# Kernel optimization log

Measured on AMD Instinct MI355X. Metric: run time of the kernel, lower is better.

Reference implementation:

```python
import jax, jax.numpy as jnp
import numpy as np
from jax import lax

N, C_IN, DIMS, NW, T, H, W = 8, 64, 64, 8, 16, 64, 64
BN_EPS = 1e-5


def setup_inputs() -> dict:
    key = jax.random.key(0)
    ks = jax.random.split(key, 10)
    # kaiming-ish scales
    w_scale = (2.0 / (C_IN * 27)) ** 0.5
    return {
        "x": jax.random.normal(ks[0], (N, C_IN, T, H, W), dtype=jnp.float32),
        "weights": jax.random.normal(ks[1], (NW, DIMS, C_IN, 3, 3, 3), dtype=jnp.float32) * w_scale,
        "biases": jax.random.normal(ks[2], (NW, DIMS), dtype=jnp.float32),
        "se_w1": jax.random.normal(ks[3], (16, C_IN, 5, 5), dtype=jnp.float32) * (2.0 / (C_IN * 25)) ** 0.5,
        "se_b1": jnp.zeros((16,), dtype=jnp.float32),
        "se_w2": jax.random.normal(ks[4], (32, 16, 5, 5), dtype=jnp.float32) * (2.0 / (16 * 25)) ** 0.5,
        "se_b2": jnp.zeros((32,), dtype=jnp.float32),
        "lin_w": jax.random.normal(ks[5], (NW, 32), dtype=jnp.float32) * (1.0 / 32) ** 0.5,
        "lin_b": jnp.zeros((NW,), dtype=jnp.float32),
        "bn_gamma": jnp.ones((DIMS,), dtype=jnp.float32),
        "bn_beta": jnp.zeros((DIMS,), dtype=jnp.float32),
        "epochs_num": 15,
    }


def _forward(x, weights, biases, se_w1, se_b1, se_w2, se_b2, lin_w, lin_b, bn_gamma, bn_beta, epochs_num):
    tau = 30.0 - 2.9 * epochs_num if epochs_num < 10 else 1.0
    # std over temporal axis (torch.std -> unbiased, ddof=1): [n, c, h, w]
    std_x = jnp.std(x, axis=2, ddof=1)
    # squeeze-expand attention branch
    dn2d = ("NCHW", "OIHW", "NCHW")
    h1 = lax.conv_general_dilated(std_x, se_w1, (1, 1), "VALID", dimension_numbers=dn2d)
    h1 = jax.nn.relu(h1 + se_b1[None, :, None, None])
    h2 = lax.conv_general_dilated(h1, se_w2, (1, 1), "VALID", dimension_numbers=dn2d)
    h2 = jax.nn.relu(h2 + se_b2[None, :, None, None])
    pooled = jnp.max(h2, axis=(2, 3))                      # [n, 32]
    logits = pooled @ lin_w.T + lin_b                       # [n, num_weights]
    phi = jax.nn.softmax(logits / tau, axis=1)
    # per-sample dynamic kernels / biases
    dyn_w = jnp.einsum("bn,ncidhw->bcidhw", phi, weights)   # [n, dims, c_in, 3,3,3]
    dyn_b = phi @ biases                                    # [n, dims]
    # grouped conv3d (groups = n) == per-sample conv3d via vmap
    dn3d = ("NCDHW", "OIDHW", "NCDHW")
    def one_conv(xi, wi):
        return lax.conv_general_dilated(xi[None], wi, (1, 1, 1), "SAME", dimension_numbers=dn3d)[0]
    y = jax.vmap(one_conv)(x, dyn_w)                        # [n, dims, t, h, w]
    y = y + dyn_b[:, :, None, None, None]
    # BatchNorm3d (training mode, batch stats, biased var)
    mean = jnp.mean(y, axis=(0, 2, 3, 4))
    var = jnp.var(y, axis=(0, 2, 3, 4))
    b = lambda v: v[None, :, None, None, None]
    y = (y - b(mean)) * b(bn_gamma) * lax.rsqrt(b(var) + BN_EPS) + b(bn_beta)
    return jax.nn.relu(y)


def reference(x, weights, biases, se_w1, se_b1, se_w2, se_b2, lin_w, lin_b, bn_gamma, bn_beta, epochs_num):
    return _forward(x, weights, biases, se_w1, se_b1, se_w2, se_b2, lin_w, lin_b, bn_gamma, bn_beta, epochs_num)
```

## Files before the change

kernel.cpp:

```cpp
#include <hip/hip_runtime.h>
#include <hip/hip_bf16.h>
#include <math.h>

#define N_   8
#define CIN_ 64
#define DIMS_ 64
#define NW_  8
#define T_   16
#define H_   64
#define W_   64
#define HW_  (H_ * W_)
#define THW_ (T_ * HW_)

typedef short bf16x8 __attribute__((ext_vector_type(8)));
typedef float f32x16 __attribute__((ext_vector_type(16)));

__device__ __forceinline__ unsigned short f2bf(float f) {
    union { float f; unsigned u; } a; a.f = f;
    unsigned r = a.u + 0x7fffu + ((a.u >> 16) & 1u);
    return (unsigned short)(r >> 16);
}
__device__ __forceinline__ float bf2f(unsigned short u) {
    union { unsigned u; float f; } a; a.u = ((unsigned)u) << 16; return a.f;
}

#define CS8_ 8
#define HS8_ (66 * CS8_)
#define TS8_ (10 * HS8_)
#define XSH_ (3 * TS8_)

__host__ __device__ constexpr int OXc(int tap) {
    int tt = tap > 26 ? 26 : tap;
    return (tt / 9) * TS8_ + ((tt % 9) / 3) * HS8_ + ((tt % 3) - 1) * CS8_;
}

__global__ __launch_bounds__(512) void stdxb_kernel(
    const float* __restrict__ x, float* __restrict__ std_x,
    unsigned short* __restrict__ xb, float* __restrict__ sums,
    unsigned* __restrict__ pooled,
    const float* __restrict__ w1, const float* __restrict__ w2,
    float* __restrict__ w1t, float* __restrict__ w2t)
{
    __shared__ unsigned short xsl[16 * 64 * 8];
    const int h = blockIdx.x, c8 = blockIdx.y, n = blockIdx.z;
    const int tid = threadIdx.x;
    const int bf = blockIdx.x + (blockIdx.y << 6) + ((int)blockIdx.z << 9);
    if (bf == 0) {
        if (tid < 128) sums[tid] = 0.f;
        else if (tid < 384) pooled[tid - 128] = 0u;
    }
    if (bf < 75) {
        int i = bf * 512 + tid;
        if (i < 25600) {
            int k = i / 1600, c = (i / 25) % 64, tap = i % 25;
            w1t[(c * 25 + tap) * 16 + k] = w1[i];
        } else if (i < 38400) {
            int j = i - 25600;
            int o = j / 400, c = (j / 25) % 16, tap = j % 25;
            w2t[(c * 25 + tap) * 32 + o] = w2[j];
        }
    }
    const int c = tid >> 6, w = tid & 63;
    const int cin = c8 * 8 + c;
    const float* px = x + (((size_t)(n * 64 + cin)) << 16) + (h << 6) + w;
    float s = 0.f, s2 = 0.f;
#pragma unroll
    for (int t = 0; t < T_; ++t) {
        float v = px[t * HW_];
        s += v;
        s2 += v * v;
        xsl[(t << 9) + (w << 3) + c] = f2bf(v);
    }
    float var = (s2 - s * s * (1.0f / 16.0f)) * (1.0f / 15.0f);
    std_x[(((size_t)(n * 64 + cin)) << 12) + (h << 6) + w] = sqrtf(fmaxf(var, 0.f));
    __syncthreads();
    const int4* src = (const int4*)xsl;
    int4* dst = (int4*)(xb + ((size_t)((n * 8 + c8) * 16) << 12) * 8);
#pragma unroll
    for (int k = 0; k < 2; ++k) {
        int j = tid + (k << 9);
        int t = j >> 6, ww = j & 63;
        dst[((t << 6) + h) * 64 + ww] = src[j];
    }
}

__global__ __launch_bounds__(256) void se_conv1c(const float* __restrict__ std_x,
        const float* __restrict__ w1t, const float* __restrict__ b1, float* __restrict__ h1) {
    __shared__ float red[3][64][8];
    const int n = blockIdx.y, ks = blockIdx.z * 8;
    const int iq = threadIdx.x & 63, cq = threadIdx.x >> 6;
    const int ij = blockIdx.x * 64 + iq;
    float acc[8];
#pragma unroll
    for (int q = 0; q < 8; ++q) acc[q] = 0.f;
    if (ij < 3600) {
        int i = ij / 60, j = ij - i * 60;
        const float* xn = std_x + (size_t)n * CIN_ * HW_ + i * W_ + j;
        for (int c = cq * 16; c < cq * 16 + 16; ++c) {
            const float* xc = xn + c * HW_;
            float xv[25];
#pragma unroll
            for (int u = 0; u < 5; ++u)
#pragma unroll
                for (int v = 0; v < 5; ++v) xv[u * 5 + v] = xc[u * W_ + v];
            const float* wc = w1t + c * 400 + ks;
#pragma unroll
            for (int tap = 0; tap < 25; ++tap)
#pragma unroll
                for (int q = 0; q < 8; ++q)
                    acc[q] = fmaf(xv[tap], wc[tap * 16 + q], acc[q]);
        }
    }
    if (cq > 0) {
#pragma unroll
        for (int q = 0; q < 8; ++q) red[cq - 1][iq][q] = acc[q];
    }
    __syncthreads();
    if (cq == 0 && ij < 3600) {
#pragma unroll
        for (int q = 0; q < 8; ++q) {
            float a = acc[q] + red[0][iq][q] + red[1][iq][q] + red[2][iq][q] + b1[ks + q];
            h1[((size_t)(n * 16 + ks + q)) * 3600 + ij] = fmaxf(a, 0.f);
        }
    }
}

__global__ __launch_bounds__(256) void se_conv2c(const float* __restrict__ h1,
        const float* __restrict__ w2t, const float* __restrict__ b2,
        unsigned* __restrict__ pooled) {
    __shared__ float red[3][64][8];
    const int n = blockIdx.y, os = blockIdx.z * 8;
    const int iq = threadIdx.x & 63, cq = threadIdx.x >> 6;
    const int ij = blockIdx.x * 64 + iq;
    const int i = ij / 56, j = ij - i * 56;
    float acc[8];
#pragma unroll
    for (int q = 0; q < 8; ++q) acc[q] = 0.f;
    const float* xn = h1 + (size_t)n * 16 * 3600 + i * 60 + j;
    for (int c = cq * 4; c < cq * 4 + 4; ++c) {
        const float* xc = xn + c * 3600;
        float xv[25];
#pragma unroll
        for (int u = 0; u < 5; ++u)
#pragma unroll
            for (int v = 0; v < 5; ++v) xv[u * 5 + v] = xc[u * 60 + v];
        const float* wc = w2t + c * 800 + os;
#pragma unroll
        for (int tap = 0; tap < 25; ++tap)
#pragma unroll
            for (int q = 0; q < 8; ++q)
                acc[q] = fmaf(xv[tap], wc[tap * 32 + q], acc[q]);
    }
    if (cq > 0) {
#pragma unroll
        for (int q = 0; q < 8; ++q) red[cq - 1][iq][q] = acc[q];
    }
    __syncthreads();
    if (cq == 0) {
#pragma unroll
        for (int q = 0; q < 8; ++q) {
            float a = fmaxf(acc[q] + red[0][iq][q] + red[1][iq][q] + red[2][iq][q] + b2[os + q], 0.f);
#pragma unroll
            for (int m = 1; m < 64; m <<= 1) a = fmaxf(a, __shfl_xor(a, m, 64));
            if (iq == 0) atomicMax(&pooled[n * 32 + os + q], __float_as_uint(a));
        }
    }
}

__global__ __launch_bounds__(256) void dyn_w_head(
    const float* __restrict__ weights, const float* __restrict__ pooled,
    const float* __restrict__ lin_w, const float* __restrict__ lin_b,
    const float* __restrict__ biases, const int* __restrict__ epochs,
    unsigned short* __restrict__ wtb2, float* __restrict__ dyn_b) {
    __shared__ float slog[8][8];
    __shared__ float sphi[64];
    const int tid = threadIdx.x;
    const int e = epochs[0];
    const float tau = (e < 10) ? (30.0f - 2.9f * (float)e) : 1.0f;
    if (tid < 64) {
        int b = tid >> 3, m = tid & 7;
        float acc = lin_b[m];
#pragma unroll
        for (int k = 0; k < 32; ++k) acc += pooled[b * 32 + k] * lin_w[m * 32 + k];
        slog[b][m] = acc / tau;
    }
    __syncthreads();
    if (tid < 8) {
        float mx = slog[tid][0];
#pragma unroll
        for (int m = 1; m < 8; ++m) mx = fmaxf(mx, slog[tid][m]);
        float ex[8], ssum = 0.f;
#pragma unroll
        for (int m = 0; m < 8; ++m) { ex[m] = expf(slog[tid][m] - mx); ssum += ex[m]; }
        float inv = 1.0f / ssum;
#pragma unroll
        for (int m = 0; m < 8; ++m) sphi[tid * 8 + m] = ex[m] * inv;
    }
    __syncthreads();
    if (blockIdx.x < 64) {
        int b = blockIdx.x >> 3, c8 = blockIdx.x & 7;
        unsigned* dst = (unsigned*)(wtb2 + (size_t)b * 114688 + (size_t)(c8 * 28 + 27) * 512);
        dst[tid] = 0u;
    }
    if (blockIdx.x == 0) {
#pragma unroll
        for (int idx = tid; idx < 512; idx += 256) {
            int b = idx >> 6, d = idx & 63;
            float a = 0.f;
#pragma unroll
            for (int m = 0; m < 8; ++m) a += sphi[b * 8 + m] * biases[m * DIMS_ + d];
            dyn_b[idx] = a;
        }
    }
    int f = blockIdx.x * 256 + tid;
    if (f >= 110592) return;
    int tap = f % 27, cin = (f / 27) & 63, co = f / 1728;
    float wv[8];
#pragma unroll
    for (int m = 0; m < 8; ++m) wv[m] = weights[(size_t)m * 110592 + f];
    size_t dbase = (size_t)(cin >> 3) * 14336 + tap * 512 + co * 8 + (cin & 7);
#pragma unroll
    for (int b = 0; b < 8; ++b) {
        float acc = 0.f;
#pragma unroll
        for (int m = 0; m < 8; ++m) acc += sphi[b * 8 + m] * wv[m];
        wtb2[(size_t)b * 114688 + dbase] = f2bf(acc);
    }
}

__global__ __launch_bounds__(256, 2) void conv3d_mfma8(
    const unsigned short* __restrict__ xb,
    const unsigned short* __restrict__ wtb2,
    const float* __restrict__ dynb,
    float* __restrict__ y,
    unsigned short* __restrict__ ybf,
    float* __restrict__ sums)
{
    __shared__ __align__(16) unsigned short xs[XSH_];
    __shared__ float bnred[128];

    const int hb = blockIdx.x, t = blockIdx.y, n = blockIdx.z;
    const int tid = threadIdx.x;
    const int lane = tid & 63, wid = tid >> 6;
    const int lane31 = lane & 31, tau = lane >> 5;
    const int hbase = hb * 8;

    for (int i = tid; i < XSH_ / 8; i += 256)
        *(int4*)&xs[i * 8] = (int4){0, 0, 0, 0};
    if (tid < 128) bnred[tid] = 0.f;

    const unsigned short* xnb = xb + (size_t)n * 4194304;
    const unsigned short* wnb = wtb2 + (size_t)n * 114688;

    f32x16 acc[2][4];
#pragma unroll
    for (int ci = 0; ci < 2; ++ci)
#pragma unroll
        for (int s = 0; s < 4; ++s)
            acc[ci][s] = (f32x16)(0.f);

    const int aBase = tau * 512 + lane31 * 8;
    int bsp[4];
#pragma unroll
    for (int s = 0; s < 4; ++s)
        bsp[s] = (2 * wid + (s >> 1)) * HS8_ + (1 + (s & 1) * 32 + lane31) * CS8_;

    for (int c8 = 0; c8 < 8; ++c8) {
        __syncthreads();
#pragma unroll
        for (int k = 0; k < 8; ++k) {
            int r = wid + (k << 2);
            if (r < 30) {
                int tp = (r >= 20) ? 2 : (r >= 10 ? 1 : 0);
                int hp = r - tp * 10;
                int gt = t + tp - 1, gh = hbase + hp - 1;
                if (((unsigned)gt < 16u) && ((unsigned)gh < 64u)) {
                    const unsigned short* gp = xnb + (size_t)(((c8 * 16 + gt) * 64 + gh) * 64 + lane) * 8;
                    const unsigned short* lp = &xs[tp * TS8_ + hp * HS8_ + CS8_];
                    __builtin_amdgcn_global_load_lds(
                        (const __attribute__((address_space(1))) void*)gp,
                        (__attribute__((address_space(3))) void*)lp, 16, 0, 0);
                }
            }
        }
        __syncthreads();

        const unsigned short* wA = wnb + (size_t)c8 * 14336;
#pragma unroll
        for (int p = 0; p < 14; ++p) {
            const int xo = tau ? OXc(2 * p + 1) : OXc(2 * p);
            bf16x8 a0 = *(const bf16x8*)(wA + p * 1024 + aBase);
            bf16x8 a1 = *(const bf16x8*)(wA + p * 1024 + aBase + 256);
            bf16x8 b0 = *(const bf16x8*)&xs[bsp[0] + xo];
            bf16x8 b1 = *(const bf16x8*)&xs[bsp[1] + xo];
            bf16x8 b2 = *(const bf16x8*)&xs[bsp[2] + xo];
            bf16x8 b3 = *(const bf16x8*)&xs[bsp[3] + xo];
            acc[0][0] = __builtin_amdgcn_mfma_f32_32x32x16_bf16(a0, b0, acc[0][0], 0, 0, 0);
            acc[0][1] = __builtin_amdgcn_mfma_f32_32x32x16_bf16(a0, b1, acc[0][1], 0, 0, 0);
            acc[0][2] = __builtin_amdgcn_mfma_f32_32x32x16_bf16(a0, b2, acc[0][2], 0, 0, 0);
            acc[0][3] = __builtin_amdgcn_mfma_f32_32x32x16_bf16(a0, b3, acc[0][3], 0, 0, 0);
            acc[1][0] = __builtin_amdgcn_mfma_f32_32x32x16_bf16(a1, b0, acc[1][0], 0, 0, 0);
            acc[1][1] = __builtin_amdgcn_mfma_f32_32x32x16_bf16(a1, b1, acc[1][1], 0, 0, 0);
            acc[1][2] = __builtin_amdgcn_mfma_f32_32x32x16_bf16(a1, b2, acc[1][2], 0, 0, 0);
            acc[1][3] = __builtin_amdgcn_mfma_f32_32x32x16_bf16(a1, b3, acc[1][3], 0, 0, 0);
        }
    }

    const float* db = dynb + n * DIMS_;
    const bool bf = (ybf != nullptr);
#pragma unroll
    for (int ci = 0; ci < 2; ++ci) {
#pragma unroll
        for (int r = 0; r < 16; ++r) {
            const int co = 32 * ci + (r & 3) + 8 * (r >> 2) + 4 * tau;
            const float bco = db[co];
            float ps = 0.f, ps2 = 0.f;
#pragma unroll
            for (int s = 0; s < 4; ++s) {
                float z = acc[ci][s][r] + bco;
                size_t yi = ((size_t)(n * 64 + co) << 16) + ((size_t)t << 12)
                          + ((size_t)(hbase + 2 * wid + (s >> 1)) << 6) + (s & 1) * 32 + lane31;
                if (bf) ybf[yi] = f2bf(z);
                else    y[yi] = z;
                ps += z;
                ps2 += z * z;
            }
#pragma unroll
            for (int m = 1; m < 32; m <<= 1) {
                ps += __shfl_xor(ps, m, 64);
                ps2 += __shfl_xor(ps2, m, 64);
            }
            if (lane31 == 0) {
                atomicAdd(&bnred[co], ps);
                atomicAdd(&bnred[64 + co], ps2);
            }
        }
    }
    __syncthreads();
    if (tid < 128) atomicAdd(&sums[tid], bnred[tid]);
}

__global__ void bn_norm_bf(const float* __restrict__ sums, const float* __restrict__ gamma,
                           const float* __restrict__ beta,
                           const unsigned short* __restrict__ ybf, float* __restrict__ out) {
    const float cnt = (float)(N_ * THW_);
    for (size_t i8 = (size_t)blockIdx.x * 256 + threadIdx.x; i8 < 4194304;
         i8 += (size_t)4096 * 256) {
        int c = (int)((i8 >> 13) & 63);
        float mean = sums[c] / cnt;
        float var = sums[64 + c] / cnt - mean * mean;
        float sc = gamma[c] * rsqrtf(var + 1e-5f);
        float sh = beta[c] - mean * sc;
        int4 raw = ((const int4*)ybf)[i8];
        const unsigned short* u = (const unsigned short*)&raw;
        float4 o0, o1;
        o0.x = fmaxf(fmaf(bf2f(u[0]), sc, sh), 0.f);
        o0.y = fmaxf(fmaf(bf2f(u[1]), sc, sh), 0.f);
        o0.z = fmaxf(fmaf(bf2f(u[2]), sc, sh), 0.f);
        o0.w = fmaxf(fmaf(bf2f(u[3]), sc, sh), 0.f);
        o1.x = fmaxf(fmaf(bf2f(u[4]), sc, sh), 0.f);
        o1.y = fmaxf(fmaf(bf2f(u[5]), sc, sh), 0.f);
        o1.z = fmaxf(fmaf(bf2f(u[6]), sc, sh), 0.f);
        o1.w = fmaxf(fmaf(bf2f(u[7]), sc, sh), 0.f);
        ((float4*)out)[i8 * 2]     = o0;
        ((float4*)out)[i8 * 2 + 1] = o1;
    }
}

__global__ void bn_norm4(const float* __restrict__ sums, const float* __restrict__ gamma,
                         const float* __restrict__ beta, float* __restrict__ y) {
    const float cnt = (float)(N_ * THW_);
    for (size_t idx = (size_t)blockIdx.x * 256 + threadIdx.x; idx < 8388608;
         idx += (size_t)4096 * 256) {
        int c = (int)((idx >> 14) & 63);
        float mean = sums[c] / cnt;
        float var = sums[64 + c] / cnt - mean * mean;
        float sc = gamma[c] * rsqrtf(var + 1e-5f);
        float sh = beta[c] - mean * sc;
        float4 v = ((float4*)y)[idx];
        v.x = fmaxf(fmaf(v.x, sc, sh), 0.f);
        v.y = fmaxf(fmaf(v.y, sc, sh), 0.f);
        v.z = fmaxf(fmaf(v.z, sc, sh), 0.f);
        v.w = fmaxf(fmaf(v.w, sc, sh), 0.f);
        ((float4*)y)[idx] = v;
    }
}

extern "C" void kernel_launch(void* const* d_in, const int* in_sizes, int n_in,
                              void* d_out, int out_size, void* d_ws, size_t ws_size,
                              hipStream_t stream) {
    const float* x       = (const float*)d_in[0];
    const float* weights = (const float*)d_in[1];
    const float* biases  = (const float*)d_in[2];
    const float* se_w1   = (const float*)d_in[3];
    const float* se_b1   = (const float*)d_in[4];
    const float* se_w2   = (const float*)d_in[5];
    const float* se_b2   = (const float*)d_in[6];
    const float* lin_w   = (const float*)d_in[7];
    const float* lin_b   = (const float*)d_in[8];
    const float* gamma   = (const float*)d_in[9];
    const float* beta    = (const float*)d_in[10];
    const int*   epochs  = (const int*)d_in[11];

    float* out = (float*)d_out;
    float* ws = (float*)d_ws;

    const size_t STD_OFF  = 0;
    const size_t H1_OFF   = STD_OFF + 2097152;
    const size_t SUMS_OFF = H1_OFF + 460800;
    const size_t POOL_OFF = SUMS_OFF + 128;
    const size_t PHI_OFF  = POOL_OFF + 256;
    const size_t DYNB_OFF = PHI_OFF + 64;
    const size_t WTB_OFF  = DYNB_OFF + 512;
    const size_t W1T_OFF  = WTB_OFF + 458752;
    const size_t W2T_OFF  = W1T_OFF + 25600;
    const size_t XB_OFF   = W2T_OFF + 12800;
    const size_t YBF_OFF  = XB_OFF + 16777216;
    const size_t NEEDED   = (YBF_OFF + 16777216) * 4;

    float* std_x  = ws + STD_OFF;
    float* h1     = ws + H1_OFF;
    float* sums   = ws + SUMS_OFF;
    float* pooled = ws + POOL_OFF;
    float* dynb   = ws + DYNB_OFF;
    unsigned short* wtb2 = (unsigned short*)(ws + WTB_OFF);
    float* w1t    = ws + W1T_OFF;
    float* w2t    = ws + W2T_OFF;
    unsigned short* xb = (unsigned short*)(ws + XB_OFF);
    unsigned short* ybf = (unsigned short*)(ws + YBF_OFF);

    const bool bf_path = (ws_size >= NEEDED);

    stdxb_kernel<<<dim3(64, 8, 8), 512, 0, stream>>>(
        x, std_x, xb, sums, (unsigned*)pooled, se_w1, se_w2, w1t, w2t);

    se_conv1c<<<dim3(57, 8, 2), 256, 0, stream>>>(std_x, w1t, se_b1, h1);
    se_conv2c<<<dim3(49, 8, 4), 256, 0, stream>>>(h1, w2t, se_b2, (unsigned*)pooled);

    dyn_w_head<<<432, 256, 0, stream>>>(weights, pooled, lin_w, lin_b, biases, epochs,
                                        wtb2, dynb);

    conv3d_mfma8<<<dim3(8, 16, 8), 256, 0, stream>>>(
        xb, wtb2, dynb, out, bf_path ? ybf : nullptr, sums);

    if (bf_path)
        bn_norm_bf<<<4096, 256, 0, stream>>>(sums, gamma, beta, ybf, out);
    else
        bn_norm4<<<4096, 256, 0, stream>>>(sums, gamma, beta, out);
}
```

Measured before the change: 377.6 us.

## Stage conv weights in LDS, remap block order, use nontemporal BN I/O

```diff
diff --git a/kernel.cpp b/kernel.cpp
--- a/kernel.cpp
+++ b/kernel.cpp
@@ -14,6 +14,8 @@
 
 typedef short bf16x8 __attribute__((ext_vector_type(8)));
 typedef float f32x16 __attribute__((ext_vector_type(16)));
+typedef int   i32x4v __attribute__((ext_vector_type(4)));
+typedef float f32x4v __attribute__((ext_vector_type(4)));
 
 __device__ __forceinline__ unsigned short f2bf(float f) {
     union { float f; unsigned u; } a; a.f = f;
@@ -28,6 +30,7 @@
 #define HS8_ (66 * CS8_)
 #define TS8_ (10 * HS8_)
 #define XSH_ (3 * TS8_)
+#define WLH_ (28 * 64 * 8)
 
 __host__ __device__ constexpr int OXc(int tap) {
     int tt = tap > 26 ? 26 : tap;
@@ -228,7 +231,7 @@
     }
 }
 
-__global__ __launch_bounds__(256, 2) void conv3d_mfma8(
+__global__ __launch_bounds__(256, 2) void conv3d_mfma5(
     const unsigned short* __restrict__ xb,
     const unsigned short* __restrict__ wtb2,
     const float* __restrict__ dynb,
@@ -237,9 +240,13 @@
     float* __restrict__ sums)
 {
     __shared__ __align__(16) unsigned short xs[XSH_];
+    __shared__ __align__(16) unsigned short wl[WLH_];
     __shared__ float bnred[128];
 
-    const int hb = blockIdx.x, t = blockIdx.y, n = blockIdx.z;
+    const int flat = blockIdx.x;
+    const int n = flat & 7;
+    const int hb = (flat >> 3) & 7;
+    const int t = flat >> 6;
     const int tid = threadIdx.x;
     const int lane = tid & 63, wid = tid >> 6;
     const int lane31 = lane & 31, tau = lane >> 5;
@@ -267,6 +274,15 @@
 
     for (int c8 = 0; c8 < 8; ++c8) {
         __syncthreads();
+#pragma unroll
+        for (int k = 0; k < 7; ++k) {
+            int tp = wid + (k << 2);
+            const unsigned short* gp = wnb + ((size_t)c8 * 14336 + tp * 512 + lane * 8);
+            const unsigned short* lp = &wl[tp * 512];
+            __builtin_amdgcn_global_load_lds(
+                (const __attribute__((address_space(1))) void*)gp,
+                (__attribute__((address_space(3))) void*)lp, 16, 0, 0);
+        }
 #pragma unroll
         for (int k = 0; k < 8; ++k) {
             int r = wid + (k << 2);
@@ -285,12 +301,11 @@
         }
         __syncthreads();
 
-        const unsigned short* wA = wnb + (size_t)c8 * 14336;
 #pragma unroll
         for (int p = 0; p < 14; ++p) {
             const int xo = tau ? OXc(2 * p + 1) : OXc(2 * p);
-            bf16x8 a0 = *(const bf16x8*)(wA + p * 1024 + aBase);
-            bf16x8 a1 = *(const bf16x8*)(wA + p * 1024 + aBase + 256);
+            bf16x8 a0 = *(const bf16x8*)&wl[p * 1024 + aBase];
+            bf16x8 a1 = *(const bf16x8*)&wl[p * 1024 + aBase + 256];
             bf16x8 b0 = *(const bf16x8*)&xs[bsp[0] + xo];
             bf16x8 b1 = *(const bf16x8*)&xs[bsp[1] + xo];
             bf16x8 b2 = *(const bf16x8*)&xs[bsp[2] + xo];
@@ -351,9 +366,9 @@
         float var = sums[64 + c] / cnt - mean * mean;
         float sc = gamma[c] * rsqrtf(var + 1e-5f);
         float sh = beta[c] - mean * sc;
-        int4 raw = ((const int4*)ybf)[i8];
+        i32x4v raw = __builtin_nontemporal_load((const i32x4v*)ybf + i8);
         const unsigned short* u = (const unsigned short*)&raw;
-        float4 o0, o1;
+        f32x4v o0, o1;
         o0.x = fmaxf(fmaf(bf2f(u[0]), sc, sh), 0.f);
         o0.y = fmaxf(fmaf(bf2f(u[1]), sc, sh), 0.f);
         o0.z = fmaxf(fmaf(bf2f(u[2]), sc, sh), 0.f);
@@ -362,8 +377,8 @@
         o1.y = fmaxf(fmaf(bf2f(u[5]), sc, sh), 0.f);
         o1.z = fmaxf(fmaf(bf2f(u[6]), sc, sh), 0.f);
         o1.w = fmaxf(fmaf(bf2f(u[7]), sc, sh), 0.f);
-        ((float4*)out)[i8 * 2]     = o0;
-        ((float4*)out)[i8 * 2 + 1] = o1;
+        __builtin_nontemporal_store(o0, (f32x4v*)out + i8 * 2);
+        __builtin_nontemporal_store(o1, (f32x4v*)out + i8 * 2 + 1);
     }
 }
 
@@ -440,7 +455,7 @@
     dyn_w_head<<<432, 256, 0, stream>>>(weights, pooled, lin_w, lin_b, biases, epochs,
                                         wtb2, dynb);
 
-    conv3d_mfma8<<<dim3(8, 16, 8), 256, 0, stream>>>(
+    conv3d_mfma5<<<1024, 256, 0, stream>>>(
         xb, wtb2, dynb, out, bf_path ? ybf : nullptr, sums);
 
     if (bf_path)
```

Result: no change. 373.5 us (-1.1%).
